# Optimization experiments

Measured on AMD Instinct MI355X. Metric: run time of the kernel, lower is better.

The kernel has to match this reference:

```python
import jax, jax.numpy as jnp
import numpy as np

N_NODES = 100000
N_EDGES = 640000
IN_DIM = 128
HIDDEN = 256
OUT_DIM = 64


def setup_inputs() -> dict:
    key = jax.random.key(0)
    k_x, k_e, k_w1, k_b1, k_w2, k_b2 = jax.random.split(key, 6)
    x = jax.random.normal(k_x, (N_NODES, IN_DIM), dtype=jnp.float32)
    edge_index = jax.random.randint(k_e, (2, N_EDGES), 0, N_NODES, dtype=jnp.int32)
    # torch Linear init ~ U(-1/sqrt(fan_in), 1/sqrt(fan_in)); scale here is arbitrary for a correctness baseline
    s1 = 1.0 / np.sqrt(2 * IN_DIM)
    s2 = 1.0 / np.sqrt(HIDDEN)
    W1 = jax.random.uniform(k_w1, (2 * IN_DIM, HIDDEN), minval=-s1, maxval=s1, dtype=jnp.float32)
    b1 = jax.random.uniform(k_b1, (HIDDEN,), minval=-s1, maxval=s1, dtype=jnp.float32)
    W2 = jax.random.uniform(k_w2, (HIDDEN, OUT_DIM), minval=-s2, maxval=s2, dtype=jnp.float32)
    b2 = jax.random.uniform(k_b2, (OUT_DIM,), minval=-s2, maxval=s2, dtype=jnp.float32)
    return {"x": x, "edge_index": edge_index, "W1": W1, "b1": b1, "W2": W2, "b2": b2}


def reference(x, edge_index, W1, b1, W2, b2):
    # gather source/destination node features: [E, in_dim] each
    src = x[edge_index[0]]
    dst = x[edge_index[1]]
    h = jnp.concatenate([src, dst], axis=-1)      # [E, 2*in_dim]
    h = jax.nn.relu(h @ W1 + b1)                  # [E, hidden]
    return h @ W2 + b2                            # [E, out_dim]
```

## Files before the change

kernel.cpp:

```cpp
#include <hip/hip_runtime.h>
#include <hip/hip_bf16.h>


#define N_EDGES_C 640000
#define N_NODES_C 100000
#define IN_DIM_C  128
#define CAT_DIM_C 256
#define HIDDEN_C  256
#define OUT_DIM_C 64
#define EPB       128
#define GRID_MAIN (N_EDGES_C / EPB)

typedef __attribute__((ext_vector_type(8))) short bf16x8;
typedef __attribute__((ext_vector_type(4))) float f32x4;

__device__ __forceinline__ ushort f2bs(float f) {
  union { __hip_bfloat16 h; ushort u; } c;
  c.h = __float2bfloat16(f);
  return c.u;
}

__global__ __launch_bounds__(256) void cast_x_kernel(const float* __restrict__ x,
                                                     ushort* __restrict__ xb) {
  const int i = blockIdx.x * 256 + threadIdx.x;
  const float4 v0 = reinterpret_cast<const float4*>(x)[2 * i];
  const float4 v1 = reinterpret_cast<const float4*>(x)[2 * i + 1];
  uint4 o;
  o.x = (unsigned)f2bs(v0.x) | ((unsigned)f2bs(v0.y) << 16);
  o.y = (unsigned)f2bs(v0.z) | ((unsigned)f2bs(v0.w) << 16);
  o.z = (unsigned)f2bs(v1.x) | ((unsigned)f2bs(v1.y) << 16);
  o.w = (unsigned)f2bs(v1.z) | ((unsigned)f2bs(v1.w) << 16);
  reinterpret_cast<uint4*>(xb)[i] = o;
}

__global__ __launch_bounds__(256) void prep_w_kernel(const float* __restrict__ W1,
                                                     const float* __restrict__ W2,
                                                     ushort* __restrict__ W1t,
                                                     ushort* __restrict__ W2t) {
  const int i = blockIdx.x * 256 + threadIdx.x;
  if (i < HIDDEN_C * CAT_DIM_C) {
    const int n = i >> 8, k = i & 255;
    W1t[i] = f2bs(W1[k * HIDDEN_C + n]);
  } else {
    const int j = i - HIDDEN_C * CAT_DIM_C;
    const int o = j >> 8, k = j & 255;
    W2t[j] = f2bs(W2[k * OUT_DIM_C + o]);
  }
}

template <int USE_XB>
__global__ __launch_bounds__(256, 2) void edge_ffn_kernel(
    const ushort* __restrict__ xb, const float* __restrict__ xf,
    const int* __restrict__ ei,
    const ushort* __restrict__ W1t, const float* __restrict__ b1,
    const ushort* __restrict__ W2t, const float* __restrict__ b2,
    float* __restrict__ out) {
  __shared__ ushort Hw[4][2][32][40];

  const int tid = threadIdx.x;
  const int l15 = tid & 15;
  const int lg  = (tid >> 4) & 3;
  const int wv  = tid >> 6;
  const int e_base = blockIdx.x * EPB + wv * 32;

  int ns[2], nd[2];
#pragma unroll
  for (int ef = 0; ef < 2; ++ef) {
    const int e = e_base + ef * 16 + l15;
    ns[ef] = ei[e];
    nd[ef] = ei[N_EDGES_C + e];
  }

  bf16x8 xfr[2][8];
#pragma unroll
  for (int ef = 0; ef < 2; ++ef) {
#pragma unroll
    for (int ks = 0; ks < 8; ++ks) {
      const int node = (ks < 4) ? ns[ef] : nd[ef];
      const int koff = (ks & 3) * 32 + lg * 8;
      if (USE_XB) {
        xfr[ef][ks] = *reinterpret_cast<const bf16x8*>(
            xb + (size_t)node * IN_DIM_C + koff);
      } else {
        const float4* row = reinterpret_cast<const float4*>(
            xf + (size_t)node * IN_DIM_C + koff);
        const float4 v0 = row[0];
        const float4 v1 = row[1];
        uint4 o;
        o.x = (unsigned)f2bs(v0.x) | ((unsigned)f2bs(v0.y) << 16);
        o.y = (unsigned)f2bs(v0.z) | ((unsigned)f2bs(v0.w) << 16);
        o.z = (unsigned)f2bs(v1.x) | ((unsigned)f2bs(v1.y) << 16);
        o.w = (unsigned)f2bs(v1.z) | ((unsigned)f2bs(v1.w) << 16);
        xfr[ef][ks] = *reinterpret_cast<const bf16x8*>(&o);
      }
    }
  }

  f32x4 b2v[4];
#pragma unroll
  for (int of = 0; of < 4; ++of)
    b2v[of] = *reinterpret_cast<const f32x4*>(b2 + of * 16 + lg * 4);

  f32x4 acc2[4][2];
#pragma unroll
  for (int of = 0; of < 4; ++of)
#pragma unroll
    for (int ef = 0; ef < 2; ++ef) acc2[of][ef] = (f32x4){0.f, 0.f, 0.f, 0.f};

#pragma unroll
  for (int nb = 0; nb < 8; ++nb) {
    f32x4 acc1[2][2];
#pragma unroll
    for (int np = 0; np < 2; ++np)
#pragma unroll
      for (int ef = 0; ef < 2; ++ef) acc1[np][ef] = (f32x4){0.f, 0.f, 0.f, 0.f};

#pragma unroll
    for (int np = 0; np < 2; ++np) {
      const ushort* wrow = W1t + (size_t)(nb * 32 + np * 16 + l15) * CAT_DIM_C + lg * 8;
#pragma unroll
      for (int ks = 0; ks < 8; ++ks) {
        const bf16x8 wf = *reinterpret_cast<const bf16x8*>(wrow + ks * 32);
        acc1[np][0] = __builtin_amdgcn_mfma_f32_16x16x32_bf16(wf, xfr[0][ks], acc1[np][0], 0, 0, 0);
        acc1[np][1] = __builtin_amdgcn_mfma_f32_16x16x32_bf16(wf, xfr[1][ks], acc1[np][1], 0, 0, 0);
      }
    }

#pragma unroll
    for (int np = 0; np < 2; ++np) {
      const f32x4 b1q = *reinterpret_cast<const f32x4*>(b1 + nb * 32 + np * 16 + lg * 4);
#pragma unroll
      for (int ef = 0; ef < 2; ++ef) {
        float v0 = acc1[np][ef][0] + b1q[0];
        float v1 = acc1[np][ef][1] + b1q[1];
        float v2 = acc1[np][ef][2] + b1q[2];
        float v3 = acc1[np][ef][3] + b1q[3];
        v0 = v0 > 0.f ? v0 : 0.f;
        v1 = v1 > 0.f ? v1 : 0.f;
        v2 = v2 > 0.f ? v2 : 0.f;
        v3 = v3 > 0.f ? v3 : 0.f;
        uint2 u;
        u.x = (unsigned)f2bs(v0) | ((unsigned)f2bs(v1) << 16);
        u.y = (unsigned)f2bs(v2) | ((unsigned)f2bs(v3) << 16);
        *reinterpret_cast<uint2*>(&Hw[wv][nb & 1][ef * 16 + l15][np * 16 + lg * 4]) = u;
      }
    }

    bf16x8 hfrag[2];
#pragma unroll
    for (int ef = 0; ef < 2; ++ef)
      hfrag[ef] = *reinterpret_cast<const bf16x8*>(&Hw[wv][nb & 1][ef * 16 + l15][lg * 8]);
#pragma unroll
    for (int of = 0; of < 4; ++of) {
      const bf16x8 w2f = *reinterpret_cast<const bf16x8*>(
          W2t + (size_t)(of * 16 + l15) * HIDDEN_C + nb * 32 + lg * 8);
#pragma unroll
      for (int ef = 0; ef < 2; ++ef)
        acc2[of][ef] = __builtin_amdgcn_mfma_f32_16x16x32_bf16(w2f, hfrag[ef], acc2[of][ef], 0, 0, 0);
    }
  }

#pragma unroll
  for (int ef = 0; ef < 2; ++ef) {
    const size_t erow = (size_t)(e_base + ef * 16 + l15) * OUT_DIM_C;
#pragma unroll
    for (int of = 0; of < 4; ++of) {
      f32x4 v;
      v[0] = acc2[of][ef][0] + b2v[of][0];
      v[1] = acc2[of][ef][1] + b2v[of][1];
      v[2] = acc2[of][ef][2] + b2v[of][2];
      v[3] = acc2[of][ef][3] + b2v[of][3];
      *reinterpret_cast<f32x4*>(out + erow + of * 16 + lg * 4) = v;
    }
  }
}

extern "C" void kernel_launch(void* const* d_in, const int* in_sizes, int n_in,
                              void* d_out, int out_size, void* d_ws, size_t ws_size,
                              hipStream_t stream) {
  const float* x  = (const float*)d_in[0];
  const int*   ei = (const int*)d_in[1];
  const float* W1 = (const float*)d_in[2];
  const float* b1 = (const float*)d_in[3];
  const float* W2 = (const float*)d_in[4];
  const float* b2 = (const float*)d_in[5];
  float* out = (float*)d_out;

  const size_t xb_elems  = (size_t)N_NODES_C * IN_DIM_C;
  const size_t w1t_elems = HIDDEN_C * CAT_DIM_C;
  const size_t w2t_elems = OUT_DIM_C * HIDDEN_C;
  const size_t need_full = (xb_elems + w1t_elems + w2t_elems) * sizeof(ushort);

  ushort* base = (ushort*)d_ws;
  if (ws_size >= need_full) {
    ushort* xbp = base;
    ushort* W1t = xbp + xb_elems;
    ushort* W2t = W1t + w1t_elems;
    cast_x_kernel<<<(N_NODES_C * IN_DIM_C) / (256 * 8), 256, 0, stream>>>(x, xbp);
    prep_w_kernel<<<(HIDDEN_C * CAT_DIM_C + OUT_DIM_C * HIDDEN_C) / 256, 256, 0, stream>>>(
        W1, W2, W1t, W2t);
    edge_ffn_kernel<1><<<GRID_MAIN, 256, 0, stream>>>(xbp, x, ei, W1t, b1, W2t, b2, out);
  } else {
    ushort* W1t = base;
    ushort* W2t = W1t + w1t_elems;
    prep_w_kernel<<<(HIDDEN_C * CAT_DIM_C + OUT_DIM_C * HIDDEN_C) / 256, 256, 0, stream>>>(
        W1, W2, W1t, W2t);
    edge_ffn_kernel<0><<<GRID_MAIN, 256, 0, stream>>>(nullptr, x, ei, W1t, b1, W2t, b2, out);
  }
}
```

Before: 627.8 us.

## Pre-pack weights in MFMA fragment order and raise occupancy with priority hints

Weight preparation now writes W1 and W2 in per-lane MFMA fragment order, so each wave's weight fragment load is one contiguous 1 KB read instead of strided 16-byte rows. Launch bounds go from 2 to 4 blocks per SIMD, which limits register use to raise occupancy and hide gather latency, with some risk of spills. The MFMA sections are wrapped in s_setprio, the b2 bias load moves to the epilogue to free registers, and output stores become nontemporal so they do not pollute cache.

```diff
diff --git a/kernel.cpp b/kernel.cpp
--- a/kernel.cpp
+++ b/kernel.cpp
@@ -35,29 +35,36 @@
 
 __global__ __launch_bounds__(256) void prep_w_kernel(const float* __restrict__ W1,
                                                      const float* __restrict__ W2,
-                                                     ushort* __restrict__ W1t,
-                                                     ushort* __restrict__ W2t) {
+                                                     ushort* __restrict__ W1p,
+                                                     ushort* __restrict__ W2p) {
   const int i = blockIdx.x * 256 + threadIdx.x;
   if (i < HIDDEN_C * CAT_DIM_C) {
-    const int n = i >> 8, k = i & 255;
-    W1t[i] = f2bs(W1[k * HIDDEN_C + n]);
+    const int e = i & 7, lane = (i >> 3) & 63, blk = i >> 9;
+    const int ks = blk & 7, np = (blk >> 3) & 1, nb = blk >> 4;
+    const int row = nb * 32 + np * 16 + (lane & 15);
+    const int k   = ks * 32 + (lane >> 4) * 8 + e;
+    W1p[i] = f2bs(W1[k * HIDDEN_C + row]);
   } else {
     const int j = i - HIDDEN_C * CAT_DIM_C;
-    const int o = j >> 8, k = j & 255;
-    W2t[j] = f2bs(W2[k * OUT_DIM_C + o]);
+    const int e = j & 7, lane = (j >> 3) & 63, blk = j >> 9;
+    const int nb = blk & 7, of = blk >> 3;
+    const int o = of * 16 + (lane & 15);
+    const int k = nb * 32 + (lane >> 4) * 8 + e;
+    W2p[j] = f2bs(W2[k * OUT_DIM_C + o]);
   }
 }
 
 template <int USE_XB>
-__global__ __launch_bounds__(256, 2) void edge_ffn_kernel(
+__global__ __launch_bounds__(256, 4) void edge_ffn_kernel(
     const ushort* __restrict__ xb, const float* __restrict__ xf,
     const int* __restrict__ ei,
-    const ushort* __restrict__ W1t, const float* __restrict__ b1,
-    const ushort* __restrict__ W2t, const float* __restrict__ b2,
+    const ushort* __restrict__ W1p, const float* __restrict__ b1,
+    const ushort* __restrict__ W2p, const float* __restrict__ b2,
     float* __restrict__ out) {
   __shared__ ushort Hw[4][2][32][40];
 
   const int tid = threadIdx.x;
+  const int l   = tid & 63;
   const int l15 = tid & 15;
   const int lg  = (tid >> 4) & 3;
   const int wv  = tid >> 6;
@@ -96,11 +103,6 @@
     }
   }
 
-  f32x4 b2v[4];
-#pragma unroll
-  for (int of = 0; of < 4; ++of)
-    b2v[of] = *reinterpret_cast<const f32x4*>(b2 + of * 16 + lg * 4);
-
   f32x4 acc2[4][2];
 #pragma unroll
   for (int of = 0; of < 4; ++of)
@@ -115,16 +117,18 @@
 #pragma unroll
       for (int ef = 0; ef < 2; ++ef) acc1[np][ef] = (f32x4){0.f, 0.f, 0.f, 0.f};
 
+    __builtin_amdgcn_s_setprio(1);
 #pragma unroll
     for (int np = 0; np < 2; ++np) {
-      const ushort* wrow = W1t + (size_t)(nb * 32 + np * 16 + l15) * CAT_DIM_C + lg * 8;
+      const ushort* wbase = W1p + (size_t)(((nb * 2 + np) * 8) * 64 + l) * 8;
 #pragma unroll
       for (int ks = 0; ks < 8; ++ks) {
-        const bf16x8 wf = *reinterpret_cast<const bf16x8*>(wrow + ks * 32);
+        const bf16x8 wf = *reinterpret_cast<const bf16x8*>(wbase + (size_t)ks * 512);
         acc1[np][0] = __builtin_amdgcn_mfma_f32_16x16x32_bf16(wf, xfr[0][ks], acc1[np][0], 0, 0, 0);
         acc1[np][1] = __builtin_amdgcn_mfma_f32_16x16x32_bf16(wf, xfr[1][ks], acc1[np][1], 0, 0, 0);
       }
     }
+    __builtin_amdgcn_s_setprio(0);
 
 #pragma unroll
     for (int np = 0; np < 2; ++np) {
@@ -150,14 +154,16 @@
 #pragma unroll
     for (int ef = 0; ef < 2; ++ef)
       hfrag[ef] = *reinterpret_cast<const bf16x8*>(&Hw[wv][nb & 1][ef * 16 + l15][lg * 8]);
+    __builtin_amdgcn_s_setprio(1);
 #pragma unroll
     for (int of = 0; of < 4; ++of) {
       const bf16x8 w2f = *reinterpret_cast<const bf16x8*>(
-          W2t + (size_t)(of * 16 + l15) * HIDDEN_C + nb * 32 + lg * 8);
+          W2p + (size_t)((of * 8 + nb) * 64 + l) * 8);
 #pragma unroll
       for (int ef = 0; ef < 2; ++ef)
         acc2[of][ef] = __builtin_amdgcn_mfma_f32_16x16x32_bf16(w2f, hfrag[ef], acc2[of][ef], 0, 0, 0);
     }
+    __builtin_amdgcn_s_setprio(0);
   }
 
 #pragma unroll
@@ -165,12 +171,13 @@
     const size_t erow = (size_t)(e_base + ef * 16 + l15) * OUT_DIM_C;
 #pragma unroll
     for (int of = 0; of < 4; ++of) {
+      const f32x4 b2q = *reinterpret_cast<const f32x4*>(b2 + of * 16 + lg * 4);
       f32x4 v;
-      v[0] = acc2[of][ef][0] + b2v[of][0];
-      v[1] = acc2[of][ef][1] + b2v[of][1];
-      v[2] = acc2[of][ef][2] + b2v[of][2];
-      v[3] = acc2[of][ef][3] + b2v[of][3];
-      *reinterpret_cast<f32x4*>(out + erow + of * 16 + lg * 4) = v;
+      v[0] = acc2[of][ef][0] + b2q[0];
+      v[1] = acc2[of][ef][1] + b2q[1];
+      v[2] = acc2[of][ef][2] + b2q[2];
+      v[3] = acc2[of][ef][3] + b2q[3];
+      __builtin_nontemporal_store(v, reinterpret_cast<f32x4*>(out + erow + of * 16 + lg * 4));
     }
   }
 }
@@ -187,24 +194,24 @@
   float* out = (float*)d_out;
 
   const size_t xb_elems  = (size_t)N_NODES_C * IN_DIM_C;
-  const size_t w1t_elems = HIDDEN_C * CAT_DIM_C;
-  const size_t w2t_elems = OUT_DIM_C * HIDDEN_C;
-  const size_t need_full = (xb_elems + w1t_elems + w2t_elems) * sizeof(ushort);
+  const size_t w1p_elems = HIDDEN_C * CAT_DIM_C;
+  const size_t w2p_elems = OUT_DIM_C * HIDDEN_C;
+  const size_t need_full = (xb_elems + w1p_elems + w2p_elems) * sizeof(ushort);
 
   ushort* base = (ushort*)d_ws;
   if (ws_size >= need_full) {
     ushort* xbp = base;
-    ushort* W1t = xbp + xb_elems;
-    ushort* W2t = W1t + w1t_elems;
+    ushort* W1p = xbp + xb_elems;
+    ushort* W2p = W1p + w1p_elems;
     cast_x_kernel<<<(N_NODES_C * IN_DIM_C) / (256 * 8), 256, 0, stream>>>(x, xbp);
     prep_w_kernel<<<(HIDDEN_C * CAT_DIM_C + OUT_DIM_C * HIDDEN_C) / 256, 256, 0, stream>>>(
-        W1, W2, W1t, W2t);
-    edge_ffn_kernel<1><<<GRID_MAIN, 256, 0, stream>>>(xbp, x, ei, W1t, b1, W2t, b2, out);
+        W1, W2, W1p, W2p);
+    edge_ffn_kernel<1><<<GRID_MAIN, 256, 0, stream>>>(xbp, x, ei, W1p, b1, W2p, b2, out);
   } else {
-    ushort* W1t = base;
-    ushort* W2t = W1t + w1t_elems;
+    ushort* W1p = base;
+    ushort* W2p = W1p + w1p_elems;
     prep_w_kernel<<<(HIDDEN_C * CAT_DIM_C + OUT_DIM_C * HIDDEN_C) / 256, 256, 0, stream>>>(
-        W1, W2, W1t, W2t);
-    edge_ffn_kernel<0><<<GRID_MAIN, 256, 0, stream>>>(nullptr, x, ei, W1t, b1, W2t, b2, out);
-  }
-}
+        W1, W2, W1p, W2p);
+    edge_ffn_kernel<0><<<GRID_MAIN, 256, 0, stream>>>(nullptr, x, ei, W1p, b1, W2p, b2, out);
+  }
+}
```

Result: faster. 606.7 us (-3.4%).
